# Performance work log

Hardware: AMD Instinct MI355X
Metric: run time of the kernel (lower is better)

## Reference

```python
import jax, jax.numpy as jnp
import numpy as np

COMMITMENT_COST = 0.25


def setup_inputs() -> dict:
    key = jax.random.key(0)
    k1, k2 = jax.random.split(key)
    B, D, H, W, K = 32, 64, 64, 64, 1024
    z_e = jax.random.normal(k1, (B, D, H, W), dtype=jnp.float32)
    # codebook initialized uniform(-1/K, 1/K) as in the torch module
    embedding = jax.random.uniform(k2, (K, D), dtype=jnp.float32,
                                   minval=-1.0 / K, maxval=1.0 / K)
    return {"z_e": z_e, "embedding": embedding}


def reference(z_e, embedding):
    B, D, H, W = z_e.shape
    # [B,D,H,W] -> [N, D] with N = B*H*W
    z_flat = jnp.transpose(z_e, (0, 2, 3, 1)).reshape(-1, D)
    # squared L2 distances [N, K] via expansion (same math as torch)
    dists = (jnp.sum(z_flat * z_flat, axis=1, keepdims=True)
             + jnp.sum(embedding * embedding, axis=1)
             - 2.0 * jnp.matmul(z_flat, embedding.T))
    indices_flat = jnp.argmin(dists, axis=1)            # [N]
    z_q_flat = embedding[indices_flat]                  # gather [N, D]
    z_q = jnp.transpose(z_q_flat.reshape(B, H, W, D), (0, 3, 1, 2))
    # straight-through estimator
    z_q_st = z_e + jax.lax.stop_gradient(z_q - z_e)
    vq_loss = jnp.mean((z_q - jax.lax.stop_gradient(z_e)) ** 2)
    commitment_loss = COMMITMENT_COST * jnp.mean((z_e - jax.lax.stop_gradient(z_q)) ** 2)
    indices = indices_flat.reshape(B, H, W)
    return z_q_st, indices, vq_loss, commitment_loss
```

## Files before the change

kernel.cpp:

```cpp
#include <hip/hip_runtime.h>

#define BB 32
#define DD 64
#define HWSZ 4096
#define KK 1024
#define NPIX (BB*HWSZ)
#define NELEM (NPIX*DD)

#define IDX_OUT_OFF NELEM
#define LOSS_OFF (IDX_OUT_OFF + NPIX)

#define WS_E2    0
#define WS_EBH   4096
#define WS_EBL   (WS_EBH + KK*DD*2)
#define WS_IDX   (WS_EBL + KK*DD*2)
#define WS_LIST  (WS_IDX + NPIX*4)
#define WS_CNT   (WS_LIST + NPIX*4)
#define WS_PART  (WS_CNT + 64)
#define WS_ZROWS (WS_PART + 8192)

#define PXB 128
#define ZSTR 129

#define SHIFT 0.25f
#define BAND 2.5e-4f

typedef __attribute__((ext_vector_type(8))) short short8v;
typedef __attribute__((ext_vector_type(4))) float float4v;

__device__ __forceinline__ unsigned short bf16_rne(float f) {
    unsigned u = __float_as_uint(f);
    u += 0x7fffu + ((u >> 16) & 1u);
    return (unsigned short)(u >> 16);
}
__device__ __forceinline__ float bf16_tof(unsigned short h) {
    return __uint_as_float(((unsigned)h) << 16);
}

__device__ __forceinline__ float np_sumsq64(const float* a) {
#pragma clang fp contract(off)
    float r0=0.f,r1=0.f,r2=0.f,r3=0.f,r4=0.f,r5=0.f,r6=0.f,r7=0.f;
#pragma unroll
    for (int i = 0; i < 64; i += 8) {
        r0 += a[i+0]*a[i+0]; r1 += a[i+1]*a[i+1];
        r2 += a[i+2]*a[i+2]; r3 += a[i+3]*a[i+3];
        r4 += a[i+4]*a[i+4]; r5 += a[i+5]*a[i+5];
        r6 += a[i+6]*a[i+6]; r7 += a[i+7]*a[i+7];
    }
    return ((r0+r1)+(r2+r3))+((r4+r5)+(r6+r7));
}

__device__ __forceinline__ float np_sumsq64_lds(const float* sh) {
#pragma clang fp contract(off)
    float r0=0.f,r1=0.f,r2=0.f,r3=0.f,r4=0.f,r5=0.f,r6=0.f,r7=0.f;
#pragma unroll
    for (int i = 0; i < 64; i += 8) {
        float a0=sh[i+0],a1=sh[i+1],a2=sh[i+2],a3=sh[i+3];
        float a4=sh[i+4],a5=sh[i+5],a6=sh[i+6],a7=sh[i+7];
        r0 += a0*a0; r1 += a1*a1; r2 += a2*a2; r3 += a3*a3;
        r4 += a4*a4; r5 += a5*a5; r6 += a6*a6; r7 += a7*a7;
    }
    return ((r0+r1)+(r2+r3))+((r4+r5)+(r6+r7));
}

__device__ __forceinline__ float np_sumsq64_str(const float* sh, int stride) {
#pragma clang fp contract(off)
    float r0=0.f,r1=0.f,r2=0.f,r3=0.f,r4=0.f,r5=0.f,r6=0.f,r7=0.f;
#pragma unroll
    for (int i = 0; i < 64; i += 8) {
        float a0=sh[(i+0)*stride],a1=sh[(i+1)*stride];
        float a2=sh[(i+2)*stride],a3=sh[(i+3)*stride];
        float a4=sh[(i+4)*stride],a5=sh[(i+5)*stride];
        float a6=sh[(i+6)*stride],a7=sh[(i+7)*stride];
        r0 += a0*a0; r1 += a1*a1; r2 += a2*a2; r3 += a3*a3;
        r4 += a4*a4; r5 += a5*a5; r6 += a6*a6; r7 += a7*a7;
    }
    return ((r0+r1)+(r2+r3))+((r4+r5)+(r6+r7));
}

__global__ __launch_bounds__(256) void vq_prep(const float* __restrict__ emb,
                                               short* __restrict__ ebh,
                                               short* __restrict__ ebl,
                                               float* __restrict__ e2) {
    int t    = blockIdx.x * 256 + threadIdx.x;
    int l    = t & 63;
    int slot = t >> 6;
    int ct = slot >> 1, ks = slot & 1;
    int code  = ct*16 + (l & 15);
    int dbase = ks*32 + (l >> 4)*8;
    const float* ep = emb + (size_t)code*DD + dbase;
    short8v h, lo;
#pragma unroll
    for (int j = 0; j < 8; ++j) {
        float v = ep[j];
        unsigned short hh = bf16_rne(v);
        h[j]  = (short)hh;
        lo[j] = (short)bf16_rne(v - bf16_tof(hh));
    }
    ((short8v*)ebh)[t] = h;
    ((short8v*)ebl)[t] = lo;

    if (blockIdx.x < 4) {
        int k = blockIdx.x * 256 + threadIdx.x;
        float ek[DD];
        const float4* p = reinterpret_cast<const float4*>(emb + (size_t)k * DD);
#pragma unroll
        for (int q = 0; q < 16; ++q) {
            float4 v = p[q];
            ek[4*q+0]=v.x; ek[4*q+1]=v.y; ek[4*q+2]=v.z; ek[4*q+3]=v.w;
        }
        e2[k] = np_sumsq64(ek);
    }
}

__global__ __launch_bounds__(256, 4) void vq_main(
        const float* __restrict__ z, const float* __restrict__ emb,
        const short* __restrict__ ebh, const short* __restrict__ ebl,
        const float* __restrict__ e2,
        int* __restrict__ idx, int* __restrict__ list, int* __restrict__ cnt,
        float* __restrict__ zrows, int zcap,
        float* __restrict__ out, double* __restrict__ partial) {
    __shared__ float zsh[DD * ZSTR];
    __shared__ int   idx_loc[PXB];
    __shared__ int   flpx[128], flslot[128];
    __shared__ int   q_px[128], q_k1[128], q_k2[128];
    __shared__ int   nfl, n2c;
    __shared__ double sred[256];
    const int tid = threadIdx.x;
    const int w   = tid >> 6;
    const int l   = tid & 63;
    const int lr  = l & 15;
    const int lg  = l >> 4;
    const int b   = blockIdx.x >> 5;
    const int hw0 = (blockIdx.x & 31) * PXB;
    const float* zb = z + (size_t)b*(DD*HWSZ) + hw0;

    if (tid == 0) { nfl = 0; n2c = 0; }
    {
        const int row = tid >> 7, col = tid & 127;
#pragma unroll 8
        for (int d0 = 0; d0 < DD; d0 += 2)
            zsh[(d0+row)*ZSTR + col] = zb[(size_t)(d0+row)*HWSZ + col];
    }
    __syncthreads();

    short8v ah[2][2], al[2][2];
#pragma unroll
    for (int rt = 0; rt < 2; ++rt) {
#pragma unroll
        for (int ks = 0; ks < 2; ++ks) {
            int px = w*32 + rt*16 + lr;
            int dbase = ks*32 + lg*8;
#pragma unroll
            for (int j = 0; j < 8; ++j) {
                float v = zsh[(dbase + j)*ZSTR + px];
                unsigned short hh = bf16_rne(v);
                ah[rt][ks][j] = (short)hh;
                al[rt][ks][j] = (short)bf16_rne(v - bf16_tof(hh));
            }
        }
    }

    float b1a[2][4], b2a[2][4], b3a[2][4];
#pragma unroll
    for (int rt = 0; rt < 2; ++rt)
#pragma unroll
        for (int r = 0; r < 4; ++r) {
            b1a[rt][r] = 3.4e38f; b2a[rt][r] = 3.4e38f; b3a[rt][r] = 3.4e38f;
        }

    const short8v* EBH = (const short8v*)ebh;
    const short8v* EBL = (const short8v*)ebl;

    float4v accP[2];
    float    e2P;
    unsigned kfP;

    {
        short8v bh0 = EBH[l],  bh1 = EBH[64 + l];
        short8v bl0 = EBL[l],  bl1 = EBL[64 + l];
        e2P = e2[lr] + SHIFT;
        kfP = (unsigned)lr;
#pragma unroll
        for (int rt = 0; rt < 2; ++rt) {
            float4v acc = {0.f, 0.f, 0.f, 0.f};
            acc = __builtin_amdgcn_mfma_f32_16x16x32_bf16(ah[rt][0], bh0, acc, 0,0,0);
            acc = __builtin_amdgcn_mfma_f32_16x16x32_bf16(ah[rt][1], bh1, acc, 0,0,0);
            acc = __builtin_amdgcn_mfma_f32_16x16x32_bf16(ah[rt][0], bl0, acc, 0,0,0);
            acc = __builtin_amdgcn_mfma_f32_16x16x32_bf16(ah[rt][1], bl1, acc, 0,0,0);
            acc = __builtin_amdgcn_mfma_f32_16x16x32_bf16(al[rt][0], bh0, acc, 0,0,0);
            acc = __builtin_amdgcn_mfma_f32_16x16x32_bf16(al[rt][1], bh1, acc, 0,0,0);
            accP[rt] = acc;
        }
    }

#pragma unroll 1
    for (int ct = 1; ct < 64; ++ct) {
        int s0 = ct*128 + l;
        short8v bh0 = EBH[s0], bh1 = EBH[s0+64];
        short8v bl0 = EBL[s0], bl1 = EBL[s0+64];
        float   e2c = e2[ct*16 + lr] + SHIFT;

#pragma unroll
        for (int rt = 0; rt < 2; ++rt)
#pragma unroll
            for (int r = 0; r < 4; ++r) {
                float s = __builtin_fmaf(-2.f, accP[rt][r], e2P);
                float p = __uint_as_float(
                    (__float_as_uint(s) & ~1023u) | kfP);
                float ob1 = b1a[rt][r], ob2 = b2a[rt][r];
                b1a[rt][r] = fminf(ob1, p);
                b2a[rt][r] = __builtin_amdgcn_fmed3f(ob1, ob2, p);
                b3a[rt][r] = __builtin_amdgcn_fmed3f(ob2, b3a[rt][r], p);
            }

#pragma unroll
        for (int rt = 0; rt < 2; ++rt) {
            float4v acc = {0.f, 0.f, 0.f, 0.f};
            acc = __builtin_amdgcn_mfma_f32_16x16x32_bf16(ah[rt][0], bh0, acc, 0,0,0);
            acc = __builtin_amdgcn_mfma_f32_16x16x32_bf16(ah[rt][1], bh1, acc, 0,0,0);
            acc = __builtin_amdgcn_mfma_f32_16x16x32_bf16(ah[rt][0], bl0, acc, 0,0,0);
            acc = __builtin_amdgcn_mfma_f32_16x16x32_bf16(ah[rt][1], bl1, acc, 0,0,0);
            acc = __builtin_amdgcn_mfma_f32_16x16x32_bf16(al[rt][0], bh0, acc, 0,0,0);
            acc = __builtin_amdgcn_mfma_f32_16x16x32_bf16(al[rt][1], bh1, acc, 0,0,0);
            accP[rt] = acc;
        }
        e2P = e2c;
        kfP = (unsigned)(ct*16 + lr);
    }

#pragma unroll
    for (int rt = 0; rt < 2; ++rt)
#pragma unroll
        for (int r = 0; r < 4; ++r) {
            float s = __builtin_fmaf(-2.f, accP[rt][r], e2P);
            float p = __uint_as_float((__float_as_uint(s) & ~1023u) | kfP);
            float ob1 = b1a[rt][r], ob2 = b2a[rt][r];
            b1a[rt][r] = fminf(ob1, p);
            b2a[rt][r] = __builtin_amdgcn_fmed3f(ob1, ob2, p);
            b3a[rt][r] = __builtin_amdgcn_fmed3f(ob2, b3a[rt][r], p);
        }

#pragma unroll
    for (int rt = 0; rt < 2; ++rt) {
#pragma unroll
        for (int r = 0; r < 4; ++r) {
            float b1 = b1a[rt][r], b2 = b2a[rt][r], b3 = b3a[rt][r];
#pragma unroll
            for (int m = 1; m < 16; m <<= 1) {
                float o1 = __shfl_xor(b1, m, 64);
                float o2 = __shfl_xor(b2, m, 64);
                float o3 = __shfl_xor(b3, m, 64);
                float mx  = fmaxf(b1, o1);
                float mn2 = fminf(b2, o2);
                float n1 = fminf(b1, o1);
                float n2 = fminf(mx, mn2);
                float n3 = fminf(fminf(fmaxf(mn2, mx), fmaxf(b2, o2)),
                                 fminf(b3, o3));
                b1 = n1; b2 = n2; b3 = n3;
            }
            if (lr == 0) {
                int i1 = (int)(__float_as_uint(b1) & 1023u);
                int pxl = w*32 + rt*16 + lg*4 + r;
                int n   = b*HWSZ + hw0 + pxl;
                idx[n] = i1;
                idx_loc[pxl] = i1;
                if (b2 - b1 <= BAND) {
                    if (b3 - b1 <= BAND) {
                        int p = atomicAdd(cnt, 1);
                        list[p] = n;
                        int j = atomicAdd(&nfl, 1);
                        flpx[j] = pxl; flslot[j] = p;
                    } else {
                        int i2 = (int)(__float_as_uint(b2) & 1023u);
                        int j = atomicAdd(&n2c, 1);
                        q_px[j] = pxl; q_k1[j] = i1; q_k2[j] = i2;
                    }
                }
            }
        }
    }

    __syncthreads();
    if (tid < n2c) {
        int px = q_px[tid], k1 = q_k1[tid], k2 = q_k2[tid];
        float z2 = np_sumsq64_str(&zsh[px], ZSTR);
        const float* ep1 = emb + (size_t)k1 * DD;
        const float* ep2 = emb + (size_t)k2 * DD;
        float s1 = 0.f, s2 = 0.f;
#pragma unroll
        for (int d = 0; d < DD; ++d) {
            float zd = zsh[d*ZSTR + px];
            s1 = __builtin_fmaf(zd, ep1[d], s1);
            s2 = __builtin_fmaf(zd, ep2[d], s2);
        }
        float B1v, B2v;
        {
#pragma clang fp contract(off)
            float A1 = z2 + e2[k1]; B1v = __builtin_fmaf(-2.f, s1, A1);
            float A2 = z2 + e2[k2]; B2v = __builtin_fmaf(-2.f, s2, A2);
        }
        int win;
        if (k1 < k2) win = (B2v < B1v) ? k2 : k1;
        else         win = (B1v < B2v) ? k1 : k2;
        idx[b*HWSZ + hw0 + px] = win;
        idx_loc[px] = win;
    }

    __syncthreads();
    int nf = nfl;
    for (int j0 = 0; j0 < nf; j0 += 4) {
        int jj = j0 + (tid >> 6);
        if (jj < nf) {
            int slot = flslot[jj];
            if (slot < zcap) {
                int d = tid & 63;
                zrows[(size_t)slot*64 + d] = zsh[d*ZSTR + flpx[jj]];
            }
        }
    }
    __syncthreads();

    {
        const int px = tid & 127;
        const int dh = tid >> 7;
        const int ki = idx_loc[px];
        const float4* ep = reinterpret_cast<const float4*>(
                               emb + (size_t)ki*DD + dh*32);
        float* op = out + (size_t)b*(DD*HWSZ) + (size_t)(dh*32)*HWSZ + hw0 + px;
        float lsum = 0.f;
#pragma unroll
        for (int q = 0; q < 8; ++q) {
            float4 v = ep[q];
            int d = dh*32 + 4*q;
            float z0 = zsh[(d+0)*ZSTR + px];
            float z1 = zsh[(d+1)*ZSTR + px];
            float z2v = zsh[(d+2)*ZSTR + px];
            float z3 = zsh[(d+3)*ZSTR + px];
            op[(size_t)(4*q+0)*HWSZ] = v.x;
            op[(size_t)(4*q+1)*HWSZ] = v.y;
            op[(size_t)(4*q+2)*HWSZ] = v.z;
            op[(size_t)(4*q+3)*HWSZ] = v.w;
            float f0 = v.x - z0, f1 = v.y - z1, f2 = v.z - z2v, f3 = v.w - z3;
            lsum = __builtin_fmaf(f0, f0, lsum);
            lsum = __builtin_fmaf(f1, f1, lsum);
            lsum = __builtin_fmaf(f2, f2, lsum);
            lsum = __builtin_fmaf(f3, f3, lsum);
        }
        if (dh == 0) out[IDX_OUT_OFF + b*HWSZ + hw0 + px] = (float)ki;
        sred[tid] = (double)lsum;
    }
    __syncthreads();
#pragma unroll
    for (int sdown = 128; sdown > 0; sdown >>= 1) {
        if (tid < sdown) sred[tid] += sred[tid + sdown];
        __syncthreads();
    }
    if (tid == 0) partial[blockIdx.x] = sred[0];
}

__global__ __launch_bounds__(256) void vq_exact8(
        const float* __restrict__ z, const float* __restrict__ emb,
        const float* __restrict__ e2, const float* __restrict__ zrows,
        const int* __restrict__ list, const int* __restrict__ cnt,
        int zcap, int* __restrict__ idx, float* __restrict__ out,
        double* __restrict__ delta) {
    __shared__ float zsh[DD];
    __shared__ float rbv[256];
    __shared__ int   rbi[256];
    __shared__ double dred[64];
    const int tid = threadIdx.x;
    const int C   = *cnt;

    for (int i = blockIdx.x; i < C; i += gridDim.x) {
        const int n = list[i];
        if (tid < 64) {
            if (i < zcap) {
                zsh[tid] = zrows[(size_t)i*64 + tid];
            } else {
                zsh[tid] = z[(size_t)(n>>12)*(DD*HWSZ) + (n&4095)
                             + (size_t)tid*HWSZ];
            }
        }
        __syncthreads();

        const float z2 = np_sumsq64_lds(zsh);

        float bestv = 3.4e38f; int bi = 0x7fffffff;
#pragma unroll
        for (int c = 0; c < 4; ++c) {
            int k = c*256 + tid;
            const float4* ep = reinterpret_cast<const float4*>(emb + (size_t)k*DD);
            float s = 0.f;
#pragma unroll
            for (int q = 0; q < 16; ++q) {
                float4 v = ep[q];
                s = __builtin_fmaf(zsh[4*q+0], v.x, s);
                s = __builtin_fmaf(zsh[4*q+1], v.y, s);
                s = __builtin_fmaf(zsh[4*q+2], v.z, s);
                s = __builtin_fmaf(zsh[4*q+3], v.w, s);
            }
            float Bv;
            {
#pragma clang fp contract(off)
                float A = z2 + e2[k];
                Bv = __builtin_fmaf(-2.f, s, A);
            }
            if (Bv < bestv) { bestv = Bv; bi = k; }
        }

        rbv[tid] = bestv; rbi[tid] = bi;
        __syncthreads();
#pragma unroll
        for (int sdown = 128; sdown > 0; sdown >>= 1) {
            if (tid < sdown) {
                float ov = rbv[tid + sdown]; int oi = rbi[tid + sdown];
                if (ov < rbv[tid] || (ov == rbv[tid] && oi < rbi[tid])) {
                    rbv[tid] = ov; rbi[tid] = oi;
                }
            }
            __syncthreads();
        }
        const int win = rbi[0];
        const int old = idx[n];
        if (win != old) {
            const int bq = n >> 12, hw = n & 4095;
            if (tid < 64) {
                float zd = zsh[tid];
                float en = emb[(size_t)win*DD + tid];
                float eo = emb[(size_t)old*DD + tid];
                out[(size_t)bq*(DD*HWSZ) + (size_t)tid*HWSZ + hw] = en;
                float dn = en - zd, dl = eo - zd;
                dred[tid] = (double)(dn*dn) - (double)(dl*dl);
            }
            __syncthreads();
            if (tid == 0) {
                double s = 0.0;
                for (int j = 0; j < 64; ++j) s += dred[j];
                atomicAdd(delta, s);
                idx[n] = win;
                out[IDX_OUT_OFF + n] = (float)win;
            }
        }
        __syncthreads();
    }
}

__global__ __launch_bounds__(256) void vq_finalize(
        const double* __restrict__ part, const double* __restrict__ delta,
        float* __restrict__ out) {
    __shared__ double sred[256];
    int t = threadIdx.x;
    sred[t] = part[t] + part[t + 256] + part[t + 512] + part[t + 768];
    __syncthreads();
#pragma unroll
    for (int sdown = 128; sdown > 0; sdown >>= 1) {
        if (t < sdown) sred[t] += sred[t + sdown];
        __syncthreads();
    }
    if (t == 0) {
        double m = (sred[0] + *delta) / (double)NELEM;
        out[LOSS_OFF]     = (float)m;
        out[LOSS_OFF + 1] = (float)(0.25 * m);
    }
}

extern "C" void kernel_launch(void* const* d_in, const int* in_sizes, int n_in,
                              void* d_out, int out_size, void* d_ws, size_t ws_size,
                              hipStream_t stream) {
    const float* z   = (const float*)d_in[0];
    const float* emb = (const float*)d_in[1];
    float* out = (float*)d_out;
    char*  ws  = (char*)d_ws;

    float*  e2p   = (float*)(ws + WS_E2);
    short*  ebh   = (short*)(ws + WS_EBH);
    short*  ebl   = (short*)(ws + WS_EBL);
    int*    idxp  = (int*)(ws + WS_IDX);
    int*    lst   = (int*)(ws + WS_LIST);
    int*    cntp  = (int*)(ws + WS_CNT);
    double* delta = (double*)(ws + WS_CNT + 8);
    double* part  = (double*)(ws + WS_PART);
    float*  zrows = (float*)(ws + WS_ZROWS);

    long long zrem = (long long)ws_size - (long long)WS_ZROWS;
    int zcap = zrem > 0 ? (int)(zrem / 256) : 0;
    if (zcap > NPIX) zcap = NPIX;

    hipMemsetAsync(cntp, 0, 16, stream);
    vq_prep     <<<32,       256, 0, stream>>>(emb, ebh, ebl, e2p);
    vq_main     <<<NPIX/PXB, 256, 0, stream>>>(z, emb, ebh, ebl, e2p, idxp,
                                               lst, cntp, zrows, zcap,
                                               out, part);
    vq_exact8   <<<512,      256, 0, stream>>>(z, emb, e2p, zrows, lst, cntp,
                                               zcap, idxp, out, delta);
    vq_finalize <<<1,        256, 0, stream>>>(part, delta, out);
}
```

Measured before the change: 116.3 us.

## Halve pixels per block to 64 and double occupancy of main VQ kernel

Each block of the main kernel now handles 64 pixels instead of 128, with one 16-row MFMA tile per wave instead of two. Launch bounds rise to 8 blocks per CU and the grid doubles, so the partial-sum buffer and the finalize reduction grow to match. The in-block loss reduction switches from double to float shared memory. Each codebook fragment load now feeds half as many MFMAs, so per-block reuse drops in exchange for more latency hiding from extra resident waves.

```diff
diff --git a/kernel.cpp b/kernel.cpp
--- a/kernel.cpp
+++ b/kernel.cpp
@@ -17,10 +17,10 @@
 #define WS_LIST  (WS_IDX + NPIX*4)
 #define WS_CNT   (WS_LIST + NPIX*4)
 #define WS_PART  (WS_CNT + 64)
-#define WS_ZROWS (WS_PART + 8192)
-
-#define PXB 128
-#define ZSTR 129
+#define WS_ZROWS (WS_PART + 16384)
+
+#define PXB 64
+#define ZSTR 65
 
 #define SHIFT 0.25f
 #define BAND 2.5e-4f
@@ -113,7 +113,7 @@
     }
 }
 
-__global__ __launch_bounds__(256, 4) void vq_main(
+__global__ __launch_bounds__(256, 8) void vq_main(
         const float* __restrict__ z, const float* __restrict__ emb,
         const short* __restrict__ ebh, const short* __restrict__ ebl,
         const float* __restrict__ e2,
@@ -122,57 +122,52 @@
         float* __restrict__ out, double* __restrict__ partial) {
     __shared__ float zsh[DD * ZSTR];
     __shared__ int   idx_loc[PXB];
-    __shared__ int   flpx[128], flslot[128];
-    __shared__ int   q_px[128], q_k1[128], q_k2[128];
+    __shared__ int   flpx[PXB], flslot[PXB];
+    __shared__ int   q_px[PXB], q_k1[PXB], q_k2[PXB];
     __shared__ int   nfl, n2c;
-    __shared__ double sred[256];
+    __shared__ float sredf[256];
     const int tid = threadIdx.x;
     const int w   = tid >> 6;
     const int l   = tid & 63;
     const int lr  = l & 15;
     const int lg  = l >> 4;
-    const int b   = blockIdx.x >> 5;
-    const int hw0 = (blockIdx.x & 31) * PXB;
+    const int b   = blockIdx.x >> 6;
+    const int hw0 = (blockIdx.x & 63) * PXB;
     const float* zb = z + (size_t)b*(DD*HWSZ) + hw0;
 
     if (tid == 0) { nfl = 0; n2c = 0; }
     {
-        const int row = tid >> 7, col = tid & 127;
+        const int row = tid >> 6, col = tid & 63;
 #pragma unroll 8
-        for (int d0 = 0; d0 < DD; d0 += 2)
+        for (int d0 = 0; d0 < DD; d0 += 4)
             zsh[(d0+row)*ZSTR + col] = zb[(size_t)(d0+row)*HWSZ + col];
     }
     __syncthreads();
 
-    short8v ah[2][2], al[2][2];
-#pragma unroll
-    for (int rt = 0; rt < 2; ++rt) {
-#pragma unroll
-        for (int ks = 0; ks < 2; ++ks) {
-            int px = w*32 + rt*16 + lr;
-            int dbase = ks*32 + lg*8;
-#pragma unroll
-            for (int j = 0; j < 8; ++j) {
-                float v = zsh[(dbase + j)*ZSTR + px];
-                unsigned short hh = bf16_rne(v);
-                ah[rt][ks][j] = (short)hh;
-                al[rt][ks][j] = (short)bf16_rne(v - bf16_tof(hh));
-            }
-        }
-    }
-
-    float b1a[2][4], b2a[2][4], b3a[2][4];
-#pragma unroll
-    for (int rt = 0; rt < 2; ++rt)
-#pragma unroll
-        for (int r = 0; r < 4; ++r) {
-            b1a[rt][r] = 3.4e38f; b2a[rt][r] = 3.4e38f; b3a[rt][r] = 3.4e38f;
-        }
+    short8v ah[2], al[2];
+#pragma unroll
+    for (int ks = 0; ks < 2; ++ks) {
+        int px = w*16 + lr;
+        int dbase = ks*32 + lg*8;
+#pragma unroll
+        for (int j = 0; j < 8; ++j) {
+            float v = zsh[(dbase + j)*ZSTR + px];
+            unsigned short hh = bf16_rne(v);
+            ah[ks][j] = (short)hh;
+            al[ks][j] = (short)bf16_rne(v - bf16_tof(hh));
+        }
+    }
+
+    float b1a[4], b2a[4], b3a[4];
+#pragma unroll
+    for (int r = 0; r < 4; ++r) {
+        b1a[r] = 3.4e38f; b2a[r] = 3.4e38f; b3a[r] = 3.4e38f;
+    }
 
     const short8v* EBH = (const short8v*)ebh;
     const short8v* EBL = (const short8v*)ebl;
 
-    float4v accP[2];
+    float4v  accP;
     float    e2P;
     unsigned kfP;
 
@@ -181,17 +176,14 @@
         short8v bl0 = EBL[l],  bl1 = EBL[64 + l];
         e2P = e2[lr] + SHIFT;
         kfP = (unsigned)lr;
-#pragma unroll
-        for (int rt = 0; rt < 2; ++rt) {
-            float4v acc = {0.f, 0.f, 0.f, 0.f};
-            acc = __builtin_amdgcn_mfma_f32_16x16x32_bf16(ah[rt][0], bh0, acc, 0,0,0);
-            acc = __builtin_amdgcn_mfma_f32_16x16x32_bf16(ah[rt][1], bh1, acc, 0,0,0);
-            acc = __builtin_amdgcn_mfma_f32_16x16x32_bf16(ah[rt][0], bl0, acc, 0,0,0);
-            acc = __builtin_amdgcn_mfma_f32_16x16x32_bf16(ah[rt][1], bl1, acc, 0,0,0);
-            acc = __builtin_amdgcn_mfma_f32_16x16x32_bf16(al[rt][0], bh0, acc, 0,0,0);
-            acc = __builtin_amdgcn_mfma_f32_16x16x32_bf16(al[rt][1], bh1, acc, 0,0,0);
-            accP[rt] = acc;
-        }
+        float4v acc = {0.f, 0.f, 0.f, 0.f};
+        acc = __builtin_amdgcn_mfma_f32_16x16x32_bf16(ah[0], bh0, acc, 0,0,0);
+        acc = __builtin_amdgcn_mfma_f32_16x16x32_bf16(ah[1], bh1, acc, 0,0,0);
+        acc = __builtin_amdgcn_mfma_f32_16x16x32_bf16(ah[0], bl0, acc, 0,0,0);
+        acc = __builtin_amdgcn_mfma_f32_16x16x32_bf16(ah[1], bl1, acc, 0,0,0);
+        acc = __builtin_amdgcn_mfma_f32_16x16x32_bf16(al[0], bh0, acc, 0,0,0);
+        acc = __builtin_amdgcn_mfma_f32_16x16x32_bf16(al[1], bh1, acc, 0,0,0);
+        accP = acc;
     }
 
 #pragma unroll 1
@@ -202,80 +194,71 @@
         float   e2c = e2[ct*16 + lr] + SHIFT;
 
 #pragma unroll
-        for (int rt = 0; rt < 2; ++rt)
-#pragma unroll
-            for (int r = 0; r < 4; ++r) {
-                float s = __builtin_fmaf(-2.f, accP[rt][r], e2P);
-                float p = __uint_as_float(
-                    (__float_as_uint(s) & ~1023u) | kfP);
-                float ob1 = b1a[rt][r], ob2 = b2a[rt][r];
-                b1a[rt][r] = fminf(ob1, p);
-                b2a[rt][r] = __builtin_amdgcn_fmed3f(ob1, ob2, p);
-                b3a[rt][r] = __builtin_amdgcn_fmed3f(ob2, b3a[rt][r], p);
-            }
-
-#pragma unroll
-        for (int rt = 0; rt < 2; ++rt) {
+        for (int r = 0; r < 4; ++r) {
+            float s = __builtin_fmaf(-2.f, accP[r], e2P);
+            float p = __uint_as_float((__float_as_uint(s) & ~1023u) | kfP);
+            float ob1 = b1a[r], ob2 = b2a[r];
+            b1a[r] = fminf(ob1, p);
+            b2a[r] = __builtin_amdgcn_fmed3f(ob1, ob2, p);
+            b3a[r] = __builtin_amdgcn_fmed3f(ob2, b3a[r], p);
+        }
+
+        {
             float4v acc = {0.f, 0.f, 0.f, 0.f};
-            acc = __builtin_amdgcn_mfma_f32_16x16x32_bf16(ah[rt][0], bh0, acc, 0,0,0);
-            acc = __builtin_amdgcn_mfma_f32_16x16x32_bf16(ah[rt][1], bh1, acc, 0,0,0);
-            acc = __builtin_amdgcn_mfma_f32_16x16x32_bf16(ah[rt][0], bl0, acc, 0,0,0);
-            acc = __builtin_amdgcn_mfma_f32_16x16x32_bf16(ah[rt][1], bl1, acc, 0,0,0);
-            acc = __builtin_amdgcn_mfma_f32_16x16x32_bf16(al[rt][0], bh0, acc, 0,0,0);
-            acc = __builtin_amdgcn_mfma_f32_16x16x32_bf16(al[rt][1], bh1, acc, 0,0,0);
-            accP[rt] = acc;
+            acc = __builtin_amdgcn_mfma_f32_16x16x32_bf16(ah[0], bh0, acc, 0,0,0);
+            acc = __builtin_amdgcn_mfma_f32_16x16x32_bf16(ah[1], bh1, acc, 0,0,0);
+            acc = __builtin_amdgcn_mfma_f32_16x16x32_bf16(ah[0], bl0, acc, 0,0,0);
+            acc = __builtin_amdgcn_mfma_f32_16x16x32_bf16(ah[1], bl1, acc, 0,0,0);
+            acc = __builtin_amdgcn_mfma_f32_16x16x32_bf16(al[0], bh0, acc, 0,0,0);
+            acc = __builtin_amdgcn_mfma_f32_16x16x32_bf16(al[1], bh1, acc, 0,0,0);
+            accP = acc;
         }
         e2P = e2c;
         kfP = (unsigned)(ct*16 + lr);
     }
 
 #pragma unroll
-    for (int rt = 0; rt < 2; ++rt)
-#pragma unroll
-        for (int r = 0; r < 4; ++r) {
-            float s = __builtin_fmaf(-2.f, accP[rt][r], e2P);
-            float p = __uint_as_float((__float_as_uint(s) & ~1023u) | kfP);
-            float ob1 = b1a[rt][r], ob2 = b2a[rt][r];
-            b1a[rt][r] = fminf(ob1, p);
-            b2a[rt][r] = __builtin_amdgcn_fmed3f(ob1, ob2, p);
-            b3a[rt][r] = __builtin_amdgcn_fmed3f(ob2, b3a[rt][r], p);
-        }
-
-#pragma unroll
-    for (int rt = 0; rt < 2; ++rt) {
-#pragma unroll
-        for (int r = 0; r < 4; ++r) {
-            float b1 = b1a[rt][r], b2 = b2a[rt][r], b3 = b3a[rt][r];
-#pragma unroll
-            for (int m = 1; m < 16; m <<= 1) {
-                float o1 = __shfl_xor(b1, m, 64);
-                float o2 = __shfl_xor(b2, m, 64);
-                float o3 = __shfl_xor(b3, m, 64);
-                float mx  = fmaxf(b1, o1);
-                float mn2 = fminf(b2, o2);
-                float n1 = fminf(b1, o1);
-                float n2 = fminf(mx, mn2);
-                float n3 = fminf(fminf(fmaxf(mn2, mx), fmaxf(b2, o2)),
-                                 fminf(b3, o3));
-                b1 = n1; b2 = n2; b3 = n3;
-            }
-            if (lr == 0) {
-                int i1 = (int)(__float_as_uint(b1) & 1023u);
-                int pxl = w*32 + rt*16 + lg*4 + r;
-                int n   = b*HWSZ + hw0 + pxl;
-                idx[n] = i1;
-                idx_loc[pxl] = i1;
-                if (b2 - b1 <= BAND) {
-                    if (b3 - b1 <= BAND) {
-                        int p = atomicAdd(cnt, 1);
-                        list[p] = n;
-                        int j = atomicAdd(&nfl, 1);
-                        flpx[j] = pxl; flslot[j] = p;
-                    } else {
-                        int i2 = (int)(__float_as_uint(b2) & 1023u);
-                        int j = atomicAdd(&n2c, 1);
-                        q_px[j] = pxl; q_k1[j] = i1; q_k2[j] = i2;
-                    }
+    for (int r = 0; r < 4; ++r) {
+        float s = __builtin_fmaf(-2.f, accP[r], e2P);
+        float p = __uint_as_float((__float_as_uint(s) & ~1023u) | kfP);
+        float ob1 = b1a[r], ob2 = b2a[r];
+        b1a[r] = fminf(ob1, p);
+        b2a[r] = __builtin_amdgcn_fmed3f(ob1, ob2, p);
+        b3a[r] = __builtin_amdgcn_fmed3f(ob2, b3a[r], p);
+    }
+
+#pragma unroll
+    for (int r = 0; r < 4; ++r) {
+        float b1 = b1a[r], b2 = b2a[r], b3 = b3a[r];
+#pragma unroll
+        for (int m = 1; m < 16; m <<= 1) {
+            float o1 = __shfl_xor(b1, m, 64);
+            float o2 = __shfl_xor(b2, m, 64);
+            float o3 = __shfl_xor(b3, m, 64);
+            float mx  = fmaxf(b1, o1);
+            float mn2 = fminf(b2, o2);
+            float n1 = fminf(b1, o1);
+            float n2 = fminf(mx, mn2);
+            float n3 = fminf(fminf(fmaxf(mn2, mx), fmaxf(b2, o2)),
+                             fminf(b3, o3));
+            b1 = n1; b2 = n2; b3 = n3;
+        }
+        if (lr == 0) {
+            int i1 = (int)(__float_as_uint(b1) & 1023u);
+            int pxl = w*16 + lg*4 + r;
+            int n   = b*HWSZ + hw0 + pxl;
+            idx[n] = i1;
+            idx_loc[pxl] = i1;
+            if (b2 - b1 <= BAND) {
+                if (b3 - b1 <= BAND) {
+                    int p = atomicAdd(cnt, 1);
+                    list[p] = n;
+                    int j = atomicAdd(&nfl, 1);
+                    flpx[j] = pxl; flslot[j] = p;
+                } else {
+                    int i2 = (int)(__float_as_uint(b2) & 1023u);
+                    int j = atomicAdd(&n2c, 1);
+                    q_px[j] = pxl; q_k1[j] = i1; q_k2[j] = i2;
                 }
             }
         }
@@ -322,17 +305,17 @@
     __syncthreads();
 
     {
-        const int px = tid & 127;
-        const int dh = tid >> 7;
+        const int px = tid & 63;
+        const int dq = tid >> 6;
         const int ki = idx_loc[px];
         const float4* ep = reinterpret_cast<const float4*>(
-                               emb + (size_t)ki*DD + dh*32);
-        float* op = out + (size_t)b*(DD*HWSZ) + (size_t)(dh*32)*HWSZ + hw0 + px;
+                               emb + (size_t)ki*DD + dq*16);
+        float* op = out + (size_t)b*(DD*HWSZ) + (size_t)(dq*16)*HWSZ + hw0 + px;
         float lsum = 0.f;
 #pragma unroll
-        for (int q = 0; q < 8; ++q) {
+        for (int q = 0; q < 4; ++q) {
             float4 v = ep[q];
-            int d = dh*32 + 4*q;
+            int d = dq*16 + 4*q;
             float z0 = zsh[(d+0)*ZSTR + px];
             float z1 = zsh[(d+1)*ZSTR + px];
             float z2v = zsh[(d+2)*ZSTR + px];
@@ -347,16 +330,16 @@
             lsum = __builtin_fmaf(f2, f2, lsum);
             lsum = __builtin_fmaf(f3, f3, lsum);
         }
-        if (dh == 0) out[IDX_OUT_OFF + b*HWSZ + hw0 + px] = (float)ki;
-        sred[tid] = (double)lsum;
+        if (dq == 0) out[IDX_OUT_OFF + b*HWSZ + hw0 + px] = (float)ki;
+        sredf[tid] = lsum;
     }
     __syncthreads();
 #pragma unroll
     for (int sdown = 128; sdown > 0; sdown >>= 1) {
-        if (tid < sdown) sred[tid] += sred[tid + sdown];
+        if (tid < sdown) sredf[tid] += sredf[tid + sdown];
         __syncthreads();
     }
-    if (tid == 0) partial[blockIdx.x] = sred[0];
+    if (tid == 0) partial[blockIdx.x] = (double)sredf[0];
 }
 
 __global__ __launch_bounds__(256) void vq_exact8(
@@ -451,7 +434,10 @@
         float* __restrict__ out) {
     __shared__ double sred[256];
     int t = threadIdx.x;
-    sred[t] = part[t] + part[t + 256] + part[t + 512] + part[t + 768];
+    double s = 0.0;
+#pragma unroll
+    for (int i = 0; i < 8; ++i) s += part[t + 256*i];
+    sred[t] = s;
     __syncthreads();
 #pragma unroll
     for (int sdown = 128; sdown > 0; sdown >>= 1) {
```

After: 135.4 us. 16.4% more time.

## Stage codebook tiles through double-buffered LDS shared across waves

Applied to the files above, without the earlier changes.

Before this change, each of the four waves loaded the same bf16 hi/lo codebook fragments from global memory on its own in every code tile. Now each thread loads one short8 per tile into a double-buffered LDS array, and all waves read the fragments from there. The shifted e2 norms are also preloaded into LDS once. Redundant global/L2 traffic goes down, at the cost of a block-wide __syncthreads per tile, extra LDS use that may lower occupancy, and one more enlarged workspace offset.

```diff
diff --git a/kernel.cpp b/kernel.cpp
--- a/kernel.cpp
+++ b/kernel.cpp
@@ -17,7 +17,7 @@
 #define WS_LIST  (WS_IDX + NPIX*4)
 #define WS_CNT   (WS_LIST + NPIX*4)
 #define WS_PART  (WS_CNT + 64)
-#define WS_ZROWS (WS_PART + 8192)
+#define WS_ZROWS (WS_PART + 16384)
 
 #define PXB 128
 #define ZSTR 129
@@ -120,12 +120,14 @@
         int* __restrict__ idx, int* __restrict__ list, int* __restrict__ cnt,
         float* __restrict__ zrows, int zcap,
         float* __restrict__ out, double* __restrict__ partial) {
-    __shared__ float zsh[DD * ZSTR];
-    __shared__ int   idx_loc[PXB];
-    __shared__ int   flpx[128], flslot[128];
-    __shared__ int   q_px[128], q_k1[128], q_k2[128];
-    __shared__ int   nfl, n2c;
-    __shared__ double sred[256];
+    __shared__ float   zsh[DD * ZSTR];
+    __shared__ short8v sb[2][2][128];
+    __shared__ float   e2sh[KK];
+    __shared__ int     idx_loc[PXB];
+    __shared__ int     flpx[128], flslot[128];
+    __shared__ int     q_px[128], q_k1[128], q_k2[128];
+    __shared__ int     nfl, n2c;
+    __shared__ double  sred[256];
     const int tid = threadIdx.x;
     const int w   = tid >> 6;
     const int l   = tid & 63;
@@ -134,6 +136,9 @@
     const int b   = blockIdx.x >> 5;
     const int hw0 = (blockIdx.x & 31) * PXB;
     const float* zb = z + (size_t)b*(DD*HWSZ) + hw0;
+    const short8v* EBH = (const short8v*)ebh;
+    const short8v* EBL = (const short8v*)ebl;
+    const int slot = tid & 127, half = tid >> 7;
 
     if (tid == 0) { nfl = 0; n2c = 0; }
     {
@@ -142,6 +147,10 @@
         for (int d0 = 0; d0 < DD; d0 += 2)
             zsh[(d0+row)*ZSTR + col] = zb[(size_t)(d0+row)*HWSZ + col];
     }
+#pragma unroll
+    for (int i = 0; i < 4; ++i)
+        e2sh[tid + i*256] = e2[tid + i*256] + SHIFT;
+    sb[0][half][slot] = (half ? EBL : EBH)[slot];
     __syncthreads();
 
     short8v ah[2][2], al[2][2];
@@ -169,17 +178,14 @@
             b1a[rt][r] = 3.4e38f; b2a[rt][r] = 3.4e38f; b3a[rt][r] = 3.4e38f;
         }
 
-    const short8v* EBH = (const short8v*)ebh;
-    const short8v* EBL = (const short8v*)ebl;
-
-    float4v accP[2];
+    float4v  accP[2];
     float    e2P;
     unsigned kfP;
 
     {
-        short8v bh0 = EBH[l],  bh1 = EBH[64 + l];
-        short8v bl0 = EBL[l],  bl1 = EBL[64 + l];
-        e2P = e2[lr] + SHIFT;
+        short8v bh0 = sb[0][0][l], bh1 = sb[0][0][64+l];
+        short8v bl0 = sb[0][1][l], bl1 = sb[0][1][64+l];
+        e2P = e2sh[lr];
         kfP = (unsigned)lr;
 #pragma unroll
         for (int rt = 0; rt < 2; ++rt) {
@@ -196,10 +202,8 @@
 
 #pragma unroll 1
     for (int ct = 1; ct < 64; ++ct) {
-        int s0 = ct*128 + l;
-        short8v bh0 = EBH[s0], bh1 = EBH[s0+64];
-        short8v bl0 = EBL[s0], bl1 = EBL[s0+64];
-        float   e2c = e2[ct*16 + lr] + SHIFT;
+        const int buf = ct & 1;
+        short8v stg = (half ? EBL : EBH)[ct*128 + slot];
 
 #pragma unroll
         for (int rt = 0; rt < 2; ++rt)
@@ -214,18 +218,25 @@
                 b3a[rt][r] = __builtin_amdgcn_fmed3f(ob2, b3a[rt][r], p);
             }
 
-#pragma unroll
-        for (int rt = 0; rt < 2; ++rt) {
-            float4v acc = {0.f, 0.f, 0.f, 0.f};
-            acc = __builtin_amdgcn_mfma_f32_16x16x32_bf16(ah[rt][0], bh0, acc, 0,0,0);
-            acc = __builtin_amdgcn_mfma_f32_16x16x32_bf16(ah[rt][1], bh1, acc, 0,0,0);
-            acc = __builtin_amdgcn_mfma_f32_16x16x32_bf16(ah[rt][0], bl0, acc, 0,0,0);
-            acc = __builtin_amdgcn_mfma_f32_16x16x32_bf16(ah[rt][1], bl1, acc, 0,0,0);
-            acc = __builtin_amdgcn_mfma_f32_16x16x32_bf16(al[rt][0], bh0, acc, 0,0,0);
-            acc = __builtin_amdgcn_mfma_f32_16x16x32_bf16(al[rt][1], bh1, acc, 0,0,0);
-            accP[rt] = acc;
-        }
-        e2P = e2c;
+        sb[buf][half][slot] = stg;
+        __syncthreads();
+
+        {
+            short8v bh0 = sb[buf][0][l], bh1 = sb[buf][0][64+l];
+            short8v bl0 = sb[buf][1][l], bl1 = sb[buf][1][64+l];
+#pragma unroll
+            for (int rt = 0; rt < 2; ++rt) {
+                float4v acc = {0.f, 0.f, 0.f, 0.f};
+                acc = __builtin_amdgcn_mfma_f32_16x16x32_bf16(ah[rt][0], bh0, acc, 0,0,0);
+                acc = __builtin_amdgcn_mfma_f32_16x16x32_bf16(ah[rt][1], bh1, acc, 0,0,0);
+                acc = __builtin_amdgcn_mfma_f32_16x16x32_bf16(ah[rt][0], bl0, acc, 0,0,0);
+                acc = __builtin_amdgcn_mfma_f32_16x16x32_bf16(ah[rt][1], bl1, acc, 0,0,0);
+                acc = __builtin_amdgcn_mfma_f32_16x16x32_bf16(al[rt][0], bh0, acc, 0,0,0);
+                acc = __builtin_amdgcn_mfma_f32_16x16x32_bf16(al[rt][1], bh1, acc, 0,0,0);
+                accP[rt] = acc;
+            }
+        }
+        e2P = e2sh[ct*16 + lr];
         kfP = (unsigned)(ct*16 + lr);
     }
 
@@ -312,10 +323,10 @@
     for (int j0 = 0; j0 < nf; j0 += 4) {
         int jj = j0 + (tid >> 6);
         if (jj < nf) {
-            int slot = flslot[jj];
-            if (slot < zcap) {
+            int sl = flslot[jj];
+            if (sl < zcap) {
                 int d = tid & 63;
-                zrows[(size_t)slot*64 + d] = zsh[d*ZSTR + flpx[jj]];
+                zrows[(size_t)sl*64 + d] = zsh[d*ZSTR + flpx[jj]];
             }
         }
     }
```

Result: slower. 122.9 us (+5.7%).
